# Performance work log

Hardware: AMD Instinct MI355X
Metric: run time of the kernel (lower is better)

The kernel has to match this reference:

```python
import jax, jax.numpy as jnp
import numpy as np

B, S, D, H = 2, 2048, 1024, 16
Dh = D // H
LN_EPS = 1e-5


def setup_inputs() -> dict:
    key = jax.random.key(0)
    ks = jax.random.split(key, 14)
    s = 1.0 / np.sqrt(D)
    return {
        "q": jax.random.normal(ks[0], (B, S, D), jnp.float32),
        "k": jax.random.normal(ks[1], (B, S, D), jnp.float32),
        "v": jax.random.normal(ks[2], (B, S, D), jnp.float32),
        "attn_mask": jax.random.randint(ks[3], (B, S, S), 0, 2).astype(bool),
        "Wq": jax.random.normal(ks[4], (D, D), jnp.float32) * s,
        "bq": jnp.zeros((D,), jnp.float32),
        "Wk": jax.random.normal(ks[5], (D, D), jnp.float32) * s,
        "bk": jnp.zeros((D,), jnp.float32),
        "Wv": jax.random.normal(ks[6], (D, D), jnp.float32) * s,
        "bv": jnp.zeros((D,), jnp.float32),
        "Wo": jax.random.normal(ks[7], (D, D), jnp.float32) * s,
        "bo": jnp.zeros((D,), jnp.float32),
        "gamma": jnp.ones((D,), jnp.float32),
        "beta": jnp.zeros((D,), jnp.float32),
    }


def reference(q, k, v, attn_mask, Wq, bq, Wk, bk, Wv, bv, Wo, bo, gamma, beta):
    residual = q
    # projections (W stored as [in, out])
    qh = (q @ Wq + bq).reshape(B, S, H, Dh).transpose(0, 2, 1, 3)  # [B,H,S,Dh]
    kh = (k @ Wk + bk).reshape(B, S, H, Dh).transpose(0, 2, 1, 3)
    vh = (v @ Wv + bv).reshape(B, S, H, Dh).transpose(0, 2, 1, 3)
    scores = jnp.einsum("bhqd,bhkd->bhqk", qh, kh) / np.sqrt(Dh)
    scores = jnp.where(attn_mask[:, None, :, :], -1e9, scores)
    attn = jax.nn.softmax(scores, axis=-1)  # dropout is identity in eval
    context = jnp.einsum("bhqk,bhkd->bhqd", attn, vh)  # [B,H,S,Dh]
    # faithful to original bug: flat reshape WITHOUT transposing heads back
    context = context.reshape(B, S, D)
    out = context @ Wo + bo
    x = residual + out
    mu = jnp.mean(x, axis=-1, keepdims=True)
    var = jnp.var(x, axis=-1, keepdims=True)
    out = (x - mu) / jnp.sqrt(var + LN_EPS) * gamma + beta
    return out, attn
```

## Files before the change

### kernel.cpp

```cpp
#include <hip/hip_runtime.h>
#include <hip/hip_bf16.h>

typedef __attribute__((ext_vector_type(8))) short bf16x8;
typedef __attribute__((ext_vector_type(4))) float f32x4;

__device__ __forceinline__ short f2bf(float f) {
    union { float f; unsigned u; } v; v.f = f;
    unsigned r = (v.u + 0x7FFFu + ((v.u >> 16) & 1u)) >> 16;
    return (short)r;
}
__device__ __forceinline__ float bf2f(short s) {
    union { unsigned u; float f; } v; v.u = ((unsigned)(unsigned short)s) << 16;
    return v.f;
}
__device__ __forceinline__ void gll16(const void* g, void* l) {
    __builtin_amdgcn_global_load_lds(
        (const __attribute__((address_space(1))) unsigned int*)g,
        (__attribute__((address_space(3))) unsigned int*)l, 16, 0, 0);
}

#define QSCALE 0.18033688011112042f

__global__ __launch_bounds__(256) void k_prep(
    const float* __restrict__ qin, const float* __restrict__ kin, const float* __restrict__ vin,
    short* __restrict__ qbf, short* __restrict__ kbf, short* __restrict__ vbf,
    const float* __restrict__ Wq, const float* __restrict__ Wk,
    const float* __restrict__ Wv, const float* __restrict__ Wo,
    short* __restrict__ WqT, short* __restrict__ WkT,
    short* __restrict__ WvT, short* __restrict__ WoT,
    const int* __restrict__ mask, unsigned* __restrict__ mb)
{
    __shared__ int sm[8192];
    const int bid = blockIdx.x, tid = threadIdx.x;
    if (bid < 6144) {
        const float* in = bid < 2048 ? qin : (bid < 4096 ? kin : vin);
        short* out = bid < 2048 ? qbf : (bid < 4096 ? kbf : vbf);
        const long i = ((long)(bid & 2047) * 256 + tid) * 8;
        float4 f0 = *reinterpret_cast<const float4*>(&in[i]);
        float4 f1 = *reinterpret_cast<const float4*>(&in[i + 4]);
        bf16x8 v;
        v[0] = f2bf(f0.x); v[1] = f2bf(f0.y); v[2] = f2bf(f0.z); v[3] = f2bf(f0.w);
        v[4] = f2bf(f1.x); v[5] = f2bf(f1.y); v[6] = f2bf(f1.z); v[7] = f2bf(f1.w);
        *reinterpret_cast<bf16x8*>(&out[i]) = v;
    } else if (bid < 10240) {
        const int t2 = bid - 6144, which = t2 >> 10, local = t2 & 1023;
        const float* W = which == 0 ? Wq : (which == 1 ? Wk : (which == 2 ? Wv : Wo));
        short* WT = which == 0 ? WqT : (which == 1 ? WkT : (which == 2 ? WvT : WoT));
        float (*t)[33] = reinterpret_cast<float(*)[33]>(sm);
        const int rb = (local >> 5) * 32, cb = (local & 31) * 32;
        const int tr = tid >> 3, tc = (tid & 7) * 4;
        const float4 v = *reinterpret_cast<const float4*>(&W[(long)(rb + tr) * 1024 + cb + tc]);
        t[tr][tc + 0] = v.x; t[tr][tc + 1] = v.y; t[tr][tc + 2] = v.z; t[tr][tc + 3] = v.w;
        __syncthreads();
        short4 o;
        o.x = f2bf(t[tc + 0][tr]); o.y = f2bf(t[tc + 1][tr]);
        o.z = f2bf(t[tc + 2][tr]); o.w = f2bf(t[tc + 3][tr]);
        *reinterpret_cast<short4*>(&WT[(long)(cb + tr) * 1024 + rb + tc]) = o;
    } else {
        const long base = (long)(bid - 10240) * 8192;
#pragma unroll
        for (int i = 0; i < 8; ++i)
            *reinterpret_cast<int4*>(&sm[i * 1024 + tid * 4]) =
                *reinterpret_cast<const int4*>(&mask[base + i * 1024 + tid * 4]);
        __syncthreads();
        unsigned wv = 0;
#pragma unroll
        for (int j = 0; j < 32; ++j) wv |= (sm[tid * 32 + j] != 0 ? 1u : 0u) << j;
        mb[base / 32 + tid] = wv;
    }
}

__global__ __launch_bounds__(256) void k_gemm_qkv(
    const short* __restrict__ A0, const short* __restrict__ A1, const short* __restrict__ A2,
    const short* __restrict__ B0, const short* __restrict__ B1, const short* __restrict__ B2,
    const float* __restrict__ b0, const float* __restrict__ b1, const float* __restrict__ b2,
    short* __restrict__ o0, short* __restrict__ o1, short* __restrict__ o2)
{
    __shared__ short As[128 * 64];
    __shared__ short Bs[128 * 64];
    const int z = blockIdx.z;
    const short* A = z == 0 ? A0 : (z == 1 ? A1 : A2);
    const short* BT = z == 0 ? B0 : (z == 1 ? B1 : B2);
    const float* bias = z == 0 ? b0 : (z == 1 ? b1 : b2);
    short* outp = z == 0 ? o0 : (z == 1 ? o1 : o2);
    const float scale = z == 0 ? QSCALE : 1.0f;

    const int tid = threadIdx.x, w = tid >> 6, lane = tid & 63;
    const int lr = lane & 15, lg = lane >> 4;
    const int rowbase = blockIdx.y * 128, colbase = blockIdx.x * 128;
    const int wr = (w >> 1) * 64, wc = (w & 1) * 64;
    const int srow = lane >> 3, sc_ = (lane & 7) ^ srow;

    f32x4 acc[4][4] = {};

    for (int kb = 0; kb < 1024; kb += 64) {
#pragma unroll
        for (int ii = 0; ii < 4; ++ii) {
            const int rl = w * 32 + ii * 8 + srow;
            gll16(A + (long)(rowbase + rl) * 1024 + kb + sc_ * 8, &As[(w * 32 + ii * 8) * 64]);
            gll16(BT + (long)(colbase + rl) * 1024 + kb + sc_ * 8, &Bs[(w * 32 + ii * 8) * 64]);
        }
        __syncthreads();
#pragma unroll
        for (int ks = 0; ks < 2; ++ks) {
            bf16x8 a[4], bq[4];
#pragma unroll
            for (int m = 0; m < 4; ++m) {
                const int r = wr + m * 16 + lr;
                a[m] = *reinterpret_cast<const bf16x8*>(&As[r * 64 + (((ks * 4 + lg) ^ (r & 7)) << 3)]);
            }
#pragma unroll
            for (int n = 0; n < 4; ++n) {
                const int r = wc + n * 16 + lr;
                bq[n] = *reinterpret_cast<const bf16x8*>(&Bs[r * 64 + (((ks * 4 + lg) ^ (r & 7)) << 3)]);
            }
#pragma unroll
            for (int m = 0; m < 4; ++m)
#pragma unroll
                for (int n = 0; n < 4; ++n)
                    acc[m][n] = __builtin_amdgcn_mfma_f32_16x16x32_bf16(a[m], bq[n], acc[m][n], 0, 0, 0);
        }
        __syncthreads();
    }

#pragma unroll
    for (int m = 0; m < 4; ++m) {
#pragma unroll
        for (int n = 0; n < 4; ++n) {
            const int C = colbase + wc + n * 16 + lr;
            const float bv = bias[C];
            if (z != 2) {
#pragma unroll
                for (int rr = 0; rr < 4; ++rr) {
                    const int R = rowbase + wr + m * 16 + lg * 4 + rr;
                    const float val = (acc[m][n][rr] + bv) * scale;
                    const int b = R >> 11, s = R & 2047, h = C >> 6, dh = C & 63;
                    outp[(((long)(b * 16 + h) * 2048 + s) << 6) + dh] = f2bf(val);
                }
            } else {
                const int R0 = rowbase + wr + m * 16 + lg * 4;
                const int b = R0 >> 11, s0 = R0 & 2047, h = C >> 6, dh = C & 63;
                short4 o;
                o.x = f2bf(acc[m][n][0] + bv);
                o.y = f2bf(acc[m][n][1] + bv);
                o.z = f2bf(acc[m][n][2] + bv);
                o.w = f2bf(acc[m][n][3] + bv);
                *reinterpret_cast<short4*>(&outp[(((long)(b * 16 + h) * 64 + dh) << 11) + s0]) = o;
            }
        }
    }
}

__global__ __launch_bounds__(256) void k_gemm_o(
    const short* __restrict__ A, const short* __restrict__ BT,
    const float* __restrict__ bias, const float* __restrict__ resid,
    float* __restrict__ outp)
{
    __shared__ short As[64 * 64];
    __shared__ short Bs[128 * 64];
    const int tid = threadIdx.x, w = tid >> 6, lane = tid & 63;
    const int lr = lane & 15, lg = lane >> 4;
    const int rowbase = blockIdx.y * 64, colbase = blockIdx.x * 128;
    const int wr = (w >> 1) * 32, wc = (w & 1) * 64;
    const int srow = lane >> 3, sc_ = (lane & 7) ^ srow;

    f32x4 acc[2][4] = {};

    for (int kb = 0; kb < 1024; kb += 64) {
#pragma unroll
        for (int ii = 0; ii < 2; ++ii) {
            const int rl = w * 16 + ii * 8 + srow;
            gll16(A + (long)(rowbase + rl) * 1024 + kb + sc_ * 8, &As[(w * 16 + ii * 8) * 64]);
        }
#pragma unroll
        for (int ii = 0; ii < 4; ++ii) {
            const int rl = w * 32 + ii * 8 + srow;
            gll16(BT + (long)(colbase + rl) * 1024 + kb + sc_ * 8, &Bs[(w * 32 + ii * 8) * 64]);
        }
        __syncthreads();
#pragma unroll
        for (int ks = 0; ks < 2; ++ks) {
            bf16x8 a[2], bq[4];
#pragma unroll
            for (int m = 0; m < 2; ++m) {
                const int r = wr + m * 16 + lr;
                a[m] = *reinterpret_cast<const bf16x8*>(&As[r * 64 + (((ks * 4 + lg) ^ (r & 7)) << 3)]);
            }
#pragma unroll
            for (int n = 0; n < 4; ++n) {
                const int r = wc + n * 16 + lr;
                bq[n] = *reinterpret_cast<const bf16x8*>(&Bs[r * 64 + (((ks * 4 + lg) ^ (r & 7)) << 3)]);
            }
#pragma unroll
            for (int m = 0; m < 2; ++m)
#pragma unroll
                for (int n = 0; n < 4; ++n)
                    acc[m][n] = __builtin_amdgcn_mfma_f32_16x16x32_bf16(a[m], bq[n], acc[m][n], 0, 0, 0);
        }
        __syncthreads();
    }

#pragma unroll
    for (int m = 0; m < 2; ++m) {
#pragma unroll
        for (int n = 0; n < 4; ++n) {
            const int C = colbase + wc + n * 16 + lr;
            const float bv = bias[C];
#pragma unroll
            for (int rr = 0; rr < 4; ++rr) {
                const int R = rowbase + wr + m * 16 + lg * 4 + rr;
                const long idx = (long)R * 1024 + C;
                outp[idx] = acc[m][n][rr] + bv + resid[idx];
            }
        }
    }
}

__global__ __launch_bounds__(256, 4) void k_attn(
    const short* __restrict__ qh, const short* __restrict__ kh,
    const short* __restrict__ vt, const unsigned* __restrict__ mbits,
    float* __restrict__ attn_out, short* __restrict__ ctxb)
{
    const int g = blockIdx.x, xcd = g & 7, u = g >> 3;
    const int bh = u >> 2, qt = xcd * 4 + (u & 3);
    const int b = bh >> 4;
    const int tid = threadIdx.x, w = tid >> 6, lane = tid & 63;
    const int lr = lane & 15, lg = lane >> 4;
    const int irow = qt * 64 + w * 16;
    const long arow = (long)bh * 2048 + irow;

    __shared__ short KV[4][64 * 64];
    __shared__ short Ps[4][16 * 64];

    const short* qhp = qh + arow * 64;
    const short* khp = kh + (long)bh * 131072;
    const short* vtp = vt + (long)bh * 131072;
    const unsigned* mbp = mbits + (long)b * 131072 + (long)irow * 64;

    const bf16x8 aq0 = *reinterpret_cast<const bf16x8*>(&qhp[lr * 64 + lg * 8]);
    const bf16x8 aq1 = *reinterpret_cast<const bf16x8*>(&qhp[lr * 64 + 32 + lg * 8]);
    const int srow = lane >> 3, sc_ = (lane & 7) ^ srow;

    auto stage_k = [&](int buf, int ch) {
#pragma unroll
        for (int ii = 0; ii < 2; ++ii) {
            const int r0 = w * 16 + ii * 8;
            gll16(khp + (long)(ch * 64 + r0 + srow) * 64 + sc_ * 8, &KV[buf][r0 * 64]);
        }
    };
    auto stage_v = [&](int buf, int ch) {
#pragma unroll
        for (int ii = 0; ii < 2; ++ii) {
            const int r0 = w * 16 + ii * 8;
            gll16(vtp + (long)(r0 + srow) * 2048 + ch * 64 + sc_ * 8, &KV[2 + buf][r0 * 64]);
        }
    };
    auto kfrag = [&](int buf, int t, int ks) -> bf16x8 {
        const int r = t * 16 + lr;
        return *reinterpret_cast<const bf16x8*>(&KV[buf][r * 64 + (((ks * 4 + lg) ^ (r & 7)) << 3)]);
    };
    auto vfrag = [&](int buf, int gi, int ks) -> bf16x8 {
        const int r = gi * 16 + lr;
        return *reinterpret_cast<const bf16x8*>(&KV[2 + buf][r * 64 + (((ks * 4 + lg) ^ (r & 7)) << 3)]);
    };
    auto ps_write = [&](int row, int t, float p) {
        const int ch8 = (t * 2 + (lr >> 3)) ^ (row & 7);
        Ps[w][row * 64 + (ch8 << 3) + (lr & 7)] = f2bf(p);
    };

    float l[4] = {0.f, 0.f, 0.f, 0.f};
    f32x4 acc[4] = {};

    stage_k(0, 0); stage_v(0, 0);
    asm volatile("s_waitcnt vmcnt(0)" ::: "memory");
    __builtin_amdgcn_s_barrier();
    asm volatile("" ::: "memory");

    for (int ch = 0; ch < 32; ++ch) {
        const int cur = ch & 1;
        unsigned mw[4][2];
#pragma unroll
        for (int rr = 0; rr < 4; ++rr) {
            mw[rr][0] = mbp[(lg * 4 + rr) * 64 + ch * 2];
            mw[rr][1] = mbp[(lg * 4 + rr) * 64 + ch * 2 + 1];
        }
        asm volatile("" ::: "memory");
        if (ch < 31) { stage_k(cur ^ 1, ch + 1); stage_v(cur ^ 1, ch + 1); }
        asm volatile("" ::: "memory");

#pragma unroll
        for (int t = 0; t < 4; ++t) {
            f32x4 sc = {};
            sc = __builtin_amdgcn_mfma_f32_16x16x32_bf16(aq0, kfrag(cur, t, 0), sc, 0, 0, 0);
            sc = __builtin_amdgcn_mfma_f32_16x16x32_bf16(aq1, kfrag(cur, t, 1), sc, 0, 0, 0);
#pragma unroll
            for (int rr = 0; rr < 4; ++rr) {
                const bool masked = (mw[rr][t >> 1] >> (((t & 1) << 4) + lr)) & 1;
                const float p = exp2f(masked ? -1e9f : sc[rr]);
                l[rr] += p;
                ps_write(lg * 4 + rr, t, p);
            }
        }
        const bf16x8 pa0 = *reinterpret_cast<const bf16x8*>(&Ps[w][lr * 64 + (((0 * 4 + lg) ^ (lr & 7)) << 3)]);
        const bf16x8 pa1 = *reinterpret_cast<const bf16x8*>(&Ps[w][lr * 64 + (((1 * 4 + lg) ^ (lr & 7)) << 3)]);
#pragma unroll
        for (int gi = 0; gi < 4; ++gi) {
            acc[gi] = __builtin_amdgcn_mfma_f32_16x16x32_bf16(pa0, vfrag(cur, gi, 0), acc[gi], 0, 0, 0);
            acc[gi] = __builtin_amdgcn_mfma_f32_16x16x32_bf16(pa1, vfrag(cur, gi, 1), acc[gi], 0, 0, 0);
        }
        asm volatile("s_waitcnt vmcnt(0)" ::: "memory");
        __builtin_amdgcn_s_barrier();
        asm volatile("" ::: "memory");
    }

    float C[4];
#pragma unroll
    for (int rr = 0; rr < 4; ++rr) {
#pragma unroll
        for (int off = 1; off < 16; off <<= 1) l[rr] += __shfl_xor(l[rr], off, 16);
        l[rr] = fmaxf(l[rr], 1e-30f);
        C[rr] = log2f(l[rr]);
    }
#pragma unroll
    for (int gi = 0; gi < 4; ++gi)
#pragma unroll
        for (int rr = 0; rr < 4; ++rr)
            ctxb[(arow + lg * 4 + rr) * 64 + gi * 16 + lr] = f2bf(acc[gi][rr] / l[rr]);

    auto emit_chunk = [&](int ch, unsigned (&mw)[4][2]) {
        const int buf = ch & 3;
#pragma unroll
        for (int t = 0; t < 4; ++t) {
            f32x4 sc = {};
            sc = __builtin_amdgcn_mfma_f32_16x16x32_bf16(aq0, kfrag(buf, t, 0), sc, 0, 0, 0);
            sc = __builtin_amdgcn_mfma_f32_16x16x32_bf16(aq1, kfrag(buf, t, 1), sc, 0, 0, 0);
#pragma unroll
            for (int rr = 0; rr < 4; ++rr) {
                const bool masked = (mw[rr][t >> 1] >> (((t & 1) << 4) + lr)) & 1;
                const float p = exp2f((masked ? -1e9f : sc[rr]) - C[rr]);
                ps_write(lg * 4 + rr, t, p);
            }
        }
#pragma unroll
        for (int i2 = 0; i2 < 4; ++i2) {
            const int r = i2 * 4 + lg;
            const short4 p4 = *reinterpret_cast<const short4*>(
                &Ps[w][r * 64 + ((((lr >> 1)) ^ (r & 7)) << 3) + ((lr & 1) << 2)]);
            float4 o;
            o.x = bf2f(p4.x); o.y = bf2f(p4.y); o.z = bf2f(p4.z); o.w = bf2f(p4.w);
            *reinterpret_cast<float4*>(&attn_out[(arow + r) * 2048 + ch * 64 + lr * 4]) = o;
        }
    };

    stage_k(0, 0); stage_k(1, 1);
    asm volatile("s_waitcnt vmcnt(0)" ::: "memory");
    __builtin_amdgcn_s_barrier();
    asm volatile("" ::: "memory");

    for (int it = 0; it < 16; ++it) {
        const int chA = it * 2, chB = chA + 1;
        unsigned mwA[4][2], mwB[4][2];
#pragma unroll
        for (int rr = 0; rr < 4; ++rr) {
            mwA[rr][0] = mbp[(lg * 4 + rr) * 64 + chA * 2];
            mwA[rr][1] = mbp[(lg * 4 + rr) * 64 + chA * 2 + 1];
            mwB[rr][0] = mbp[(lg * 4 + rr) * 64 + chB * 2];
            mwB[rr][1] = mbp[(lg * 4 + rr) * 64 + chB * 2 + 1];
        }
        asm volatile("" ::: "memory");
        stage_k((chA + 2) & 3, (chA + 2) & 31);
        stage_k((chB + 2) & 3, (chB + 2) & 31);
        asm volatile("" ::: "memory");

        emit_chunk(chA, mwA);
        emit_chunk(chB, mwB);

        asm volatile("s_waitcnt vmcnt(8)" ::: "memory");
        __builtin_amdgcn_s_barrier();
        asm volatile("" ::: "memory");
    }
}

__global__ __launch_bounds__(256) void k_ln(const float* __restrict__ x,
    const float* __restrict__ gamma, const float* __restrict__ beta,
    float* __restrict__ out)
{
    __shared__ float red[8];
    const int r = blockIdx.x, tid = threadIdx.x;
    const float4 v = reinterpret_cast<const float4*>(x + (long)r * 1024)[tid];
    float s = v.x + v.y + v.z + v.w;
    float q2 = v.x * v.x + v.y * v.y + v.z * v.z + v.w * v.w;
#pragma unroll
    for (int off = 32; off; off >>= 1) {
        s += __shfl_xor(s, off, 64);
        q2 += __shfl_xor(q2, off, 64);
    }
    if ((tid & 63) == 0) { red[(tid >> 6) * 2] = s; red[(tid >> 6) * 2 + 1] = q2; }
    __syncthreads();
    s = red[0] + red[2] + red[4] + red[6];
    q2 = red[1] + red[3] + red[5] + red[7];
    const float mu = s * (1.0f / 1024.0f);
    const float var = q2 * (1.0f / 1024.0f) - mu * mu;
    const float rs = rsqrtf(var + 1e-5f);
    const float4 gm = reinterpret_cast<const float4*>(gamma)[tid];
    const float4 bb = reinterpret_cast<const float4*>(beta)[tid];
    float4 o;
    o.x = (v.x - mu) * rs * gm.x + bb.x;
    o.y = (v.y - mu) * rs * gm.y + bb.y;
    o.z = (v.z - mu) * rs * gm.z + bb.z;
    o.w = (v.w - mu) * rs * gm.w + bb.w;
    reinterpret_cast<float4*>(out + (long)r * 1024)[tid] = o;
}

extern "C" void kernel_launch(void* const* d_in, const int* in_sizes, int n_in,
                              void* d_out, int out_size, void* d_ws, size_t ws_size,
                              hipStream_t stream)
{
    const float* qin  = (const float*)d_in[0];
    const float* kin  = (const float*)d_in[1];
    const float* vin  = (const float*)d_in[2];
    const int*   mask = (const int*)d_in[3];
    const float* Wq = (const float*)d_in[4];
    const float* bq = (const float*)d_in[5];
    const float* Wk = (const float*)d_in[6];
    const float* bk = (const float*)d_in[7];
    const float* Wv = (const float*)d_in[8];
    const float* bv = (const float*)d_in[9];
    const float* Wo = (const float*)d_in[10];
    const float* bo = (const float*)d_in[11];
    const float* gamma = (const float*)d_in[12];
    const float* beta  = (const float*)d_in[13];

    char* ws = (char*)d_ws;
    short* WqT = (short*)(ws + (0ul  << 20));
    short* WkT = (short*)(ws + (2ul  << 20));
    short* WvT = (short*)(ws + (4ul  << 20));
    short* WoT = (short*)(ws + (6ul  << 20));
    short* qbf = (short*)(ws + (8ul  << 20));
    short* kbf = (short*)(ws + (16ul << 20));
    short* vbf = (short*)(ws + (24ul << 20));
    short* qh  = (short*)(ws + (32ul << 20));
    short* khb = (short*)(ws + (40ul << 20));
    short* vtb = (short*)(ws + (48ul << 20));
    unsigned* mb = (unsigned*)(ws + (56ul << 20));
    short* ctxb = (short*)(ws + (57ul << 20));
    float* xb   = (float*)(ws + (8ul  << 20));

    float* outLN = (float*)d_out;
    float* attnO = (float*)d_out + 4194304;

    const dim3 blk(256);
    k_prep<<<dim3(11264), blk, 0, stream>>>(qin, kin, vin, qbf, kbf, vbf,
                                            Wq, Wk, Wv, Wo, WqT, WkT, WvT, WoT, mask, mb);
    k_gemm_qkv<<<dim3(8, 32, 3), blk, 0, stream>>>(qbf, kbf, vbf, WqT, WkT, WvT,
                                                   bq, bk, bv, qh, khb, vtb);
    k_attn<<<dim3(1024), blk, 0, stream>>>(qh, khb, vtb, mb, attnO, ctxb);
    k_gemm_o<<<dim3(8, 64), blk, 0, stream>>>(ctxb, WoT, bo, qin, xb);
    k_ln<<<dim3(4096), blk, 0, stream>>>(xb, gamma, beta, outLN);
}
```

Measured before the change: 305.4 us.

## Widen attention blocks to 128 query rows with triple-buffered K/V staging

The attention kernel now runs 512-thread blocks that each cover 128 query rows, so every staged K/V tile is shared by eight waves and global K/V reads are halved. The first pass moves from double to triple buffering with a two-chunk prefetch and a relaxed vmcnt wait. Mask words are loaded as uint2 vectors, and the normalisation uses a reciprocal multiply instead of a division. The block-to-head mapping is also reordered. The costs are more LDS per block and fewer, larger blocks, which may lower occupancy and makes the hand-written waitcnt counts harder to keep correct.

```diff
diff --git a/kernel.cpp b/kernel.cpp
--- a/kernel.cpp
+++ b/kernel.cpp
@@ -216,21 +216,22 @@
     }
 }
 
-__global__ __launch_bounds__(256, 4) void k_attn(
+__global__ __launch_bounds__(512, 4) void k_attn(
     const short* __restrict__ qh, const short* __restrict__ kh,
     const short* __restrict__ vt, const unsigned* __restrict__ mbits,
     float* __restrict__ attn_out, short* __restrict__ ctxb)
 {
-    const int g = blockIdx.x, xcd = g & 7, u = g >> 3;
-    const int bh = u >> 2, qt = xcd * 4 + (u & 3);
+    const int g = blockIdx.x;
+    const int bh = (g & 7) * 4 + ((g >> 3) & 3);
+    const int qt = g >> 5;
     const int b = bh >> 4;
     const int tid = threadIdx.x, w = tid >> 6, lane = tid & 63;
     const int lr = lane & 15, lg = lane >> 4;
-    const int irow = qt * 64 + w * 16;
+    const int irow = qt * 128 + w * 16;
     const long arow = (long)bh * 2048 + irow;
 
-    __shared__ short KV[4][64 * 64];
-    __shared__ short Ps[4][16 * 64];
+    __shared__ short LK[6][64 * 64];
+    __shared__ short Ps[8][16 * 64];
 
     const short* qhp = qh + arow * 64;
     const short* khp = kh + (long)bh * 131072;
@@ -242,26 +243,20 @@
     const int srow = lane >> 3, sc_ = (lane & 7) ^ srow;
 
     auto stage_k = [&](int buf, int ch) {
-#pragma unroll
-        for (int ii = 0; ii < 2; ++ii) {
-            const int r0 = w * 16 + ii * 8;
-            gll16(khp + (long)(ch * 64 + r0 + srow) * 64 + sc_ * 8, &KV[buf][r0 * 64]);
-        }
+        const int r0 = w * 8;
+        gll16(khp + (long)(ch * 64 + r0 + srow) * 64 + sc_ * 8, &LK[buf][r0 * 64]);
     };
     auto stage_v = [&](int buf, int ch) {
-#pragma unroll
-        for (int ii = 0; ii < 2; ++ii) {
-            const int r0 = w * 16 + ii * 8;
-            gll16(vtp + (long)(r0 + srow) * 2048 + ch * 64 + sc_ * 8, &KV[2 + buf][r0 * 64]);
-        }
+        const int r0 = w * 8;
+        gll16(vtp + (long)(r0 + srow) * 2048 + ch * 64 + sc_ * 8, &LK[3 + buf][r0 * 64]);
     };
     auto kfrag = [&](int buf, int t, int ks) -> bf16x8 {
         const int r = t * 16 + lr;
-        return *reinterpret_cast<const bf16x8*>(&KV[buf][r * 64 + (((ks * 4 + lg) ^ (r & 7)) << 3)]);
+        return *reinterpret_cast<const bf16x8*>(&LK[buf][r * 64 + (((ks * 4 + lg) ^ (r & 7)) << 3)]);
     };
     auto vfrag = [&](int buf, int gi, int ks) -> bf16x8 {
         const int r = gi * 16 + lr;
-        return *reinterpret_cast<const bf16x8*>(&KV[2 + buf][r * 64 + (((ks * 4 + lg) ^ (r & 7)) << 3)]);
+        return *reinterpret_cast<const bf16x8*>(&LK[3 + buf][r * 64 + (((ks * 4 + lg) ^ (r & 7)) << 3)]);
     };
     auto ps_write = [&](int row, int t, float p) {
         const int ch8 = (t * 2 + (lr >> 3)) ^ (row & 7);
@@ -271,21 +266,20 @@
     float l[4] = {0.f, 0.f, 0.f, 0.f};
     f32x4 acc[4] = {};
 
-    stage_k(0, 0); stage_v(0, 0);
+    stage_k(0, 0); stage_v(0, 0); stage_k(1, 1); stage_v(1, 1);
     asm volatile("s_waitcnt vmcnt(0)" ::: "memory");
     __builtin_amdgcn_s_barrier();
     asm volatile("" ::: "memory");
 
+    int cur = 0, nxt = 2;
     for (int ch = 0; ch < 32; ++ch) {
-        const int cur = ch & 1;
-        unsigned mw[4][2];
-#pragma unroll
-        for (int rr = 0; rr < 4; ++rr) {
-            mw[rr][0] = mbp[(lg * 4 + rr) * 64 + ch * 2];
-            mw[rr][1] = mbp[(lg * 4 + rr) * 64 + ch * 2 + 1];
-        }
-        asm volatile("" ::: "memory");
-        if (ch < 31) { stage_k(cur ^ 1, ch + 1); stage_v(cur ^ 1, ch + 1); }
+        uint2 mw[4];
+#pragma unroll
+        for (int rr = 0; rr < 4; ++rr)
+            mw[rr] = *reinterpret_cast<const uint2*>(&mbp[(lg * 4 + rr) * 64 + ch * 2]);
+        asm volatile("" ::: "memory");
+        stage_k(nxt, (ch + 2) & 31);
+        stage_v(nxt, (ch + 2) & 31);
         asm volatile("" ::: "memory");
 
 #pragma unroll
@@ -295,7 +289,8 @@
             sc = __builtin_amdgcn_mfma_f32_16x16x32_bf16(aq1, kfrag(cur, t, 1), sc, 0, 0, 0);
 #pragma unroll
             for (int rr = 0; rr < 4; ++rr) {
-                const bool masked = (mw[rr][t >> 1] >> (((t & 1) << 4) + lr)) & 1;
+                const unsigned mwv = (t >> 1) ? mw[rr].y : mw[rr].x;
+                const bool masked = (mwv >> (((t & 1) << 4) + lr)) & 1;
                 const float p = exp2f(masked ? -1e9f : sc[rr]);
                 l[rr] += p;
                 ps_write(lg * 4 + rr, t, p);
@@ -308,9 +303,11 @@
             acc[gi] = __builtin_amdgcn_mfma_f32_16x16x32_bf16(pa0, vfrag(cur, gi, 0), acc[gi], 0, 0, 0);
             acc[gi] = __builtin_amdgcn_mfma_f32_16x16x32_bf16(pa1, vfrag(cur, gi, 1), acc[gi], 0, 0, 0);
         }
-        asm volatile("s_waitcnt vmcnt(0)" ::: "memory");
+        asm volatile("s_waitcnt vmcnt(2)" ::: "memory");
         __builtin_amdgcn_s_barrier();
         asm volatile("" ::: "memory");
+        cur = (cur == 2) ? 0 : cur + 1;
+        nxt = (nxt == 2) ? 0 : nxt + 1;
     }
 
     float C[4];
@@ -320,14 +317,15 @@
         for (int off = 1; off < 16; off <<= 1) l[rr] += __shfl_xor(l[rr], off, 16);
         l[rr] = fmaxf(l[rr], 1e-30f);
         C[rr] = log2f(l[rr]);
+        l[rr] = 1.0f / l[rr];
     }
 #pragma unroll
     for (int gi = 0; gi < 4; ++gi)
 #pragma unroll
         for (int rr = 0; rr < 4; ++rr)
-            ctxb[(arow + lg * 4 + rr) * 64 + gi * 16 + lr] = f2bf(acc[gi][rr] / l[rr]);
-
-    auto emit_chunk = [&](int ch, unsigned (&mw)[4][2]) {
+            ctxb[(arow + lg * 4 + rr) * 64 + gi * 16 + lr] = f2bf(acc[gi][rr] * l[rr]);
+
+    auto emit_chunk = [&](int ch, uint2 (&mw)[4]) {
         const int buf = ch & 3;
 #pragma unroll
         for (int t = 0; t < 4; ++t) {
@@ -336,7 +334,8 @@
             sc = __builtin_amdgcn_mfma_f32_16x16x32_bf16(aq1, kfrag(buf, t, 1), sc, 0, 0, 0);
 #pragma unroll
             for (int rr = 0; rr < 4; ++rr) {
-                const bool masked = (mw[rr][t >> 1] >> (((t & 1) << 4) + lr)) & 1;
+                const unsigned mwv = (t >> 1) ? mw[rr].y : mw[rr].x;
+                const bool masked = (mwv >> (((t & 1) << 4) + lr)) & 1;
                 const float p = exp2f((masked ? -1e9f : sc[rr]) - C[rr]);
                 ps_write(lg * 4 + rr, t, p);
             }
@@ -359,13 +358,11 @@
 
     for (int it = 0; it < 16; ++it) {
         const int chA = it * 2, chB = chA + 1;
-        unsigned mwA[4][2], mwB[4][2];
+        uint2 mwA[4], mwB[4];
 #pragma unroll
         for (int rr = 0; rr < 4; ++rr) {
-            mwA[rr][0] = mbp[(lg * 4 + rr) * 64 + chA * 2];
-            mwA[rr][1] = mbp[(lg * 4 + rr) * 64 + chA * 2 + 1];
-            mwB[rr][0] = mbp[(lg * 4 + rr) * 64 + chB * 2];
-            mwB[rr][1] = mbp[(lg * 4 + rr) * 64 + chB * 2 + 1];
+            mwA[rr] = *reinterpret_cast<const uint2*>(&mbp[(lg * 4 + rr) * 64 + chA * 2]);
+            mwB[rr] = *reinterpret_cast<const uint2*>(&mbp[(lg * 4 + rr) * 64 + chB * 2]);
         }
         asm volatile("" ::: "memory");
         stage_k((chA + 2) & 3, (chA + 2) & 31);
@@ -454,7 +451,7 @@
                                             Wq, Wk, Wv, Wo, WqT, WkT, WvT, WoT, mask, mb);
     k_gemm_qkv<<<dim3(8, 32, 3), blk, 0, stream>>>(qbf, kbf, vbf, WqT, WkT, WvT,
                                                    bq, bk, bv, qh, khb, vtb);
-    k_attn<<<dim3(1024), blk, 0, stream>>>(qh, khb, vtb, mb, attnO, ctxb);
+    k_attn<<<dim3(512), dim3(512), 0, stream>>>(qh, khb, vtb, mb, attnO, ctxb);
     k_gemm_o<<<dim3(8, 64), blk, 0, stream>>>(ctxb, WoT, bo, qin, xb);
     k_ln<<<dim3(4096), blk, 0, stream>>>(xb, gamma, beta, outLN);
 }
```

After: 330.8 us. 8.3% more time.
